# Optimization experiments

Hardware: AMD Instinct MI355X
Metric: run time of the kernel (lower is better)

The kernel has to match this reference:

```python
import jax, jax.numpy as jnp
import numpy as np

H = 16       # num_attention_heads
HKV = 4      # num_key_value_heads
D = 128      # head_dim
CHUNK = 64   # input_chunk_size
RBS = 64     # retrieval_block_size


def setup_inputs() -> dict:
    key = jax.random.key(0)
    ks = jax.random.split(key, 9)
    B, S, HID = 1, 2048, 2048
    RLEN = 2048  # retrieval_block_num * RBS = (S // CHUNK) * RBS
    inv = 0.02
    return {
        "hidden_states": jax.random.normal(ks[0], (B, S, HID), jnp.float32),
        "cos": jax.random.uniform(ks[1], (B, S, D), jnp.float32),
        "sin": jax.random.uniform(ks[2], (B, S, D), jnp.float32),
        "retrieval_k": jax.random.normal(ks[3], (B, HKV, RLEN, D), jnp.float32),
        "retrieval_v": jax.random.normal(ks[4], (B, HKV, RLEN, D), jnp.float32),
        "Wq": jax.random.normal(ks[5], (HID, H * D), jnp.float32) * inv,
        "Wk": jax.random.normal(ks[6], (HID, HKV * D), jnp.float32) * inv,
        "Wv": jax.random.normal(ks[7], (HID, HKV * D), jnp.float32) * inv,
        "Wo": jax.random.normal(ks[8], (H * D, HID), jnp.float32) * inv,
    }


def _rope(x, cos, sin):
    # x: [B, h, S, D]; cos/sin: [B, S, D] (HF apply_rotary_pos_emb, unsqueeze head dim)
    c = cos[:, None, :, :]
    s = sin[:, None, :, :]
    x1, x2 = jnp.split(x, 2, axis=-1)
    rot = jnp.concatenate([-x2, x1], axis=-1)
    return x * c + rot * s


def reference(hidden_states, cos, sin, retrieval_k, retrieval_v, Wq, Wk, Wv, Wo):
    B, S, HID = hidden_states.shape
    G = H // HKV
    scale = D ** -0.5

    q = (hidden_states @ Wq).reshape(B, S, H, D).transpose(0, 2, 1, 3)    # [B,H,S,D]
    k = (hidden_states @ Wk).reshape(B, S, HKV, D).transpose(0, 2, 1, 3)  # [B,HKV,S,D]
    v = (hidden_states @ Wv).reshape(B, S, HKV, D).transpose(0, 2, 1, 3)

    q = _rope(q, cos, sin)
    k = _rope(k, cos, sin)

    # GQA: expand kv heads
    k_full = jnp.repeat(k, G, axis=1)  # [B,H,S,D]
    v_full = jnp.repeat(v, G, axis=1)

    # ---- causal part over input keys ----
    s1 = jnp.einsum('bhqd,bhkd->bhqk', q, k_full) * scale
    causal = jnp.tril(jnp.ones((S, S), bool))
    s1 = jnp.where(causal[None, None], s1, -jnp.inf)

    # ---- retrieval part: chunk c attends retrieval block (c-1) only ----
    C = S // CHUNK
    R = retrieval_k.shape[2] // RBS
    rK = retrieval_k.reshape(B, HKV, R, RBS, D)
    rV = retrieval_v.reshape(B, HKV, R, RBS, D)
    blk_idx = jnp.clip(jnp.arange(C) - 1, 0, R - 1)          # chunk 0 masked below
    rK_sel = jnp.repeat(rK[:, :, blk_idx], G, axis=1)        # [B,H,C,RBS,D]
    rV_sel = jnp.repeat(rV[:, :, blk_idx], G, axis=1)
    qc = q.reshape(B, H, C, CHUNK, D)
    s2 = jnp.einsum('bhcqd,bhckd->bhcqk', qc, rK_sel) * scale
    valid = (jnp.arange(C) >= 1)[None, None, :, None, None]
    s2 = jnp.where(valid, s2, -jnp.inf)

    # ---- joint (numerically stable) softmax over causal + retrieval keys ----
    m1 = jnp.max(s1, axis=-1)                                # [B,H,S]
    m2 = jnp.max(s2, axis=-1).reshape(B, H, S)               # -inf for chunk 0
    m = jnp.maximum(m1, m2)
    e1 = jnp.exp(s1 - m[..., None])
    e2 = jnp.exp(s2 - m.reshape(B, H, C, CHUNK)[..., None])
    denom = e1.sum(-1) + e2.sum(-1).reshape(B, H, S)         # [B,H,S]
    o1 = jnp.einsum('bhqk,bhkd->bhqd', e1, v_full)
    o2 = jnp.einsum('bhcqk,bhckd->bhcqd', e2, rV_sel).reshape(B, H, S, D)
    attn = (o1 + o2) / denom[..., None]                      # [B,H,S,D]

    out = attn.transpose(0, 2, 1, 3).reshape(B, S, H * D)
    return out @ Wo
```

## Files before the change

### kernel.cpp

```cpp
#include <hip/hip_runtime.h>
#include <stdint.h>

#define H_    16
#define HKV_  4
#define D_    128
#define S_    2048
#define HID_  2048
#define RLEN_ 2048

typedef unsigned short u16;
typedef __attribute__((ext_vector_type(4))) float f32x4;
typedef __attribute__((ext_vector_type(16))) float f32x16;
typedef __attribute__((ext_vector_type(8))) __bf16 bf16x8;
typedef __attribute__((ext_vector_type(4))) unsigned short u16x4;
typedef __attribute__((ext_vector_type(8))) unsigned short u16x8;
typedef __attribute__((ext_vector_type(2))) unsigned int u32x2;

__device__ __forceinline__ u16 f2bf(float f) {
  union { float f; unsigned u; } v; v.f = f;
  unsigned r = v.u + 0x7FFFu + ((v.u >> 16) & 1u);
  return (u16)(r >> 16);
}
__device__ __forceinline__ float bf2f(u16 h) {
  union { unsigned u; float f; } v; v.u = ((unsigned)h) << 16;
  return v.f;
}
__device__ __forceinline__ float exp2v(float x) {
  float r; asm("v_exp_f32 %0, %1" : "=v"(r) : "v"(x)); return r;
}
__device__ __forceinline__ unsigned cvtpk(float lo, float hi) {
  unsigned r; asm("v_cvt_pk_bf16_f32 %0, %1, %2" : "=v"(r) : "v"(lo), "v"(hi)); return r;
}
__device__ __forceinline__ void pl32swap(unsigned &a, unsigned &b) {
  u32x2 r = __builtin_amdgcn_permlane32_swap(a, b, false, false);
  a = r.x; b = r.y;
}
__device__ __forceinline__ float xhalf_max(float v) {
  unsigned a = __float_as_uint(v), b = a;
  pl32swap(a, b);
  return fmaxf(__uint_as_float(a), __uint_as_float(b));
}
__device__ __forceinline__ float xhalf_add(float v) {
  unsigned a = __float_as_uint(v), b = a;
  pl32swap(a, b);
  return __uint_as_float(a) + __uint_as_float(b);
}

#define GLL(srcp, ldsp) \
  __builtin_amdgcn_global_load_lds((const __attribute__((address_space(1))) unsigned int*)(srcp), \
                                   (__attribute__((address_space(3))) unsigned int*)(ldsp), 16, 0, 0)

__global__ void k_cvt(const float* __restrict__ in, u16* __restrict__ out, int n4) {
  int i = blockIdx.x * 256 + threadIdx.x;
  if (i >= n4) return;
  float4 v = ((const float4*)in)[i];
  u16x4 o;
  o.x = f2bf(v.x); o.y = f2bf(v.y); o.z = f2bf(v.z); o.w = f2bf(v.w);
  ((u16x4*)out)[i] = o;
}

__global__ void k_transw(const float* __restrict__ in, u16* __restrict__ out, int K, int N) {
  __shared__ float tile[32][33];
  int bx = blockIdx.x * 32, by = blockIdx.y * 32;
  int tx = threadIdx.x, ty = threadIdx.y;
#pragma unroll
  for (int i = 0; i < 32; i += 8)
    tile[ty + i][tx] = in[(size_t)(by + ty + i) * N + bx + tx];
  __syncthreads();
#pragma unroll
  for (int i = 0; i < 32; i += 8)
    out[(size_t)(bx + ty + i) * K + by + tx] = f2bf(tile[tx][ty + i]);
}

__global__ __launch_bounds__(256) void k_gemm(const u16* __restrict__ A, const u16* __restrict__ Bt,
                                              u16* __restrict__ Cb, int M, int N, int K, int Khalf) {
  __shared__ __attribute__((aligned(16))) u16 As[128 * 32];
  __shared__ __attribute__((aligned(16))) u16 Bs[128 * 32];
  const int bm = blockIdx.y * 128, bn = blockIdx.x * 128;
  const int kz0 = blockIdx.z * Khalf, kz1 = kz0 + Khalf;
  u16* C = Cb + (size_t)blockIdx.z * M * N;
  const int tid = threadIdx.x, wave = tid >> 6, lane = tid & 63;
  const int wr = wave >> 1, wc = wave & 1;
  const int l15 = lane & 15, lhi = lane >> 4;
  f32x4 acc[4][4] = {};
  const u16* pA  = A  + (size_t)(bm + (tid >> 2)) * K + (tid & 3) * 8;
  const u16* pA2 = A  + (size_t)(bm + 64 + (tid >> 2)) * K + (tid & 3) * 8;
  const u16* pB  = Bt + (size_t)(bn + (tid >> 2)) * K + (tid & 3) * 8;
  const u16* pB2 = Bt + (size_t)(bn + 64 + (tid >> 2)) * K + (tid & 3) * 8;

  for (int k0 = kz0; k0 < kz1; k0 += 32) {
    __syncthreads();
    GLL(pA + k0,  As + wave * 512);
    GLL(pA2 + k0, As + 2048 + wave * 512);
    GLL(pB + k0,  Bs + wave * 512);
    GLL(pB2 + k0, Bs + 2048 + wave * 512);
    __syncthreads();
    bf16x8 af[4], bfr[4];
#pragma unroll
    for (int m = 0; m < 4; m++)
      af[m] = *(const bf16x8*)(As + (wr * 64 + m * 16 + l15) * 32 + lhi * 8);
#pragma unroll
    for (int n = 0; n < 4; n++)
      bfr[n] = *(const bf16x8*)(Bs + (wc * 64 + n * 16 + l15) * 32 + lhi * 8);
#pragma unroll
    for (int m = 0; m < 4; m++)
#pragma unroll
      for (int n = 0; n < 4; n++)
        acc[m][n] = __builtin_amdgcn_mfma_f32_16x16x32_bf16(af[m], bfr[n], acc[m][n], 0, 0, 0);
  }
  const int r0 = bm + wr * 64, c0 = bn + wc * 64;
#pragma unroll
  for (int m = 0; m < 4; m++)
#pragma unroll
    for (int n = 0; n < 4; n++) {
      int r = r0 + m * 16 + lhi * 4, cc = c0 + n * 16 + l15;
#pragma unroll
      for (int j = 0; j < 4; j++)
        C[(size_t)(r + j) * N + cc] = f2bf(acc[m][n][j]);
    }
}

__global__ void k_comb2(const u16* __restrict__ c0, const u16* __restrict__ c1,
                        float* __restrict__ out, int n8) {
  int i = blockIdx.x * 256 + threadIdx.x;
  if (i >= n8) return;
  u16x8 a = ((const u16x8*)c0)[i];
  u16x8 b = ((const u16x8*)c1)[i];
  float4 o0, o1;
  o0.x = bf2f(a[0]) + bf2f(b[0]); o0.y = bf2f(a[1]) + bf2f(b[1]);
  o0.z = bf2f(a[2]) + bf2f(b[2]); o0.w = bf2f(a[3]) + bf2f(b[3]);
  o1.x = bf2f(a[4]) + bf2f(b[4]); o1.y = bf2f(a[5]) + bf2f(b[5]);
  o1.z = bf2f(a[6]) + bf2f(b[6]); o1.w = bf2f(a[7]) + bf2f(b[7]);
  ((float4*)out)[i * 2]     = o0;
  ((float4*)out)[i * 2 + 1] = o1;
}

__global__ void k_ropeq(const u16* __restrict__ qp0, const float* __restrict__ cs,
                        const float* __restrict__ sn, u16* __restrict__ Q) {
  const u16* qp1 = qp0 + (size_t)2048 * 3072;
  int tid = threadIdx.x;
  int idx = blockIdx.x * 4 + (tid >> 6);
  int d = tid & 63;
  int h = idx >> 11, s = idx & (S_ - 1);
  size_t base = (size_t)s * 3072 + h * 128;
  float x1 = bf2f(qp0[base + d])      + bf2f(qp1[base + d]);
  float x2 = bf2f(qp0[base + d + 64]) + bf2f(qp1[base + d + 64]);
  float c1 = cs[s * D_ + d], s1v = sn[s * D_ + d];
  float c2 = cs[s * D_ + d + 64], s2v = sn[s * D_ + d + 64];
  const float sc = 0.12751744422f;
  u16* o = Q + ((size_t)h * S_ + s) * D_;
  o[d]      = f2bf((x1 * c1 - x2 * s1v) * sc);
  o[d + 64] = f2bf((x2 * c2 + x1 * s2v) * sc);
}

__global__ void k_ropekv(const u16* __restrict__ qp0, const float* __restrict__ cs,
                         const float* __restrict__ sn, u16* __restrict__ Ksw,
                         u16* __restrict__ Vt) {
  const u16* qp1 = qp0 + (size_t)2048 * 3072;
  int tid = threadIdx.x;
  int idx = blockIdx.x * 4 + (tid >> 6);
  int d = tid & 63;
  int kv = idx >> 11, s = idx & (S_ - 1);
  size_t kb = (size_t)s * 3072 + 2048 + kv * 128;
  size_t vb = kb + 512;
  float x1 = bf2f(qp0[kb + d])      + bf2f(qp1[kb + d]);
  float x2 = bf2f(qp0[kb + d + 64]) + bf2f(qp1[kb + d + 64]);
  float v1 = bf2f(qp0[vb + d])      + bf2f(qp1[vb + d]);
  float v2 = bf2f(qp0[vb + d + 64]) + bf2f(qp1[vb + d + 64]);
  float c1 = cs[s * D_ + d], s1v = sn[s * D_ + d];
  float c2 = cs[s * D_ + d + 64], s2v = sn[s * D_ + d + 64];
  u16* ko = Ksw + ((size_t)kv * S_ + s) * D_;
  int sw = (s & 7) << 3;
  ko[d ^ sw]        = f2bf(x1 * c1 - x2 * s1v);
  ko[(d + 64) ^ sw] = f2bf(x2 * c2 + x1 * s2v);
  u16* vo = Vt + (size_t)kv * D_ * S_;
  vo[(size_t)d * S_        + s] = f2bf(v1);
  vo[(size_t)(d + 64) * S_ + s] = f2bf(v2);
}

__global__ void k_retr(const float* __restrict__ rk, const float* __restrict__ rv,
                       u16* __restrict__ Krs, u16* __restrict__ Vtr) {
  int tid = threadIdx.x;
  int idx = blockIdx.x * 2 + (tid >> 7);
  int d = tid & 127;
  int kv = idx >> 11, r = idx & (RLEN_ - 1);
  size_t base = ((size_t)kv * RLEN_ + r) * D_;
  Krs[base + (d ^ ((r & 7) << 3))] = f2bf(rk[base + d]);
  Vtr[((size_t)kv * D_ + d) * RLEN_ + r] = f2bf(rv[base + d]);
}

__global__ __launch_bounds__(256) void k_attn(
    const u16* __restrict__ Q, const u16* __restrict__ Ksw, const u16* __restrict__ Vt,
    const u16* __restrict__ Krs, const u16* __restrict__ Vtr,
    u16* __restrict__ Opart, float* __restrict__ Ml) {
  __shared__ __attribute__((aligned(16))) char smem[69632];
  u16* KlB = (u16*)smem;
  u16* VlB = (u16*)(smem + 32768);
  float* mrg = (float*)smem;

  const int e = 83 - blockIdx.x, h = blockIdx.y, kvh = h >> 2;
  int c, part, np;
  if (e < 7)       { c = e;               part = 0;           np = 1; }
  else if (e < 23) { c = 7 + ((e - 7) >> 1);  part = (e - 7) & 1;  np = 2; }
  else if (e < 47) { c = 15 + (e - 23) / 3;   part = (e - 23) % 3; np = 3; }
  else if (e < 79) { c = 23 + ((e - 47) >> 2); part = (e - 47) & 3; np = 4; }
  else             { c = 31;              part = e - 79;      np = 5; }
  const int nt = (c == 0) ? 1 : (c + 2);
  const int t0 = (part * nt) / np, t1 = ((part + 1) * nt) / np;
  const int bp = h * 84 + e;

  const int tid = threadIdx.x, wave = tid >> 6, lane = tid & 63;
  const int qs = wave & 1, kp = wave >> 1;
  const int l31 = lane & 31, hf = lane >> 5;
  const int qrow = c * 64 + qs * 32 + l31;

  bf16x8 qf[8];
  {
    const u16* qp = Q + ((size_t)h * S_ + qrow) * D_ + hf * 8;
#pragma unroll
    for (int m = 0; m < 8; m++) qf[m] = *(const bf16x8*)(qp + m * 16);
  }
  float mq = -1e30f, lq = 0.f;
  f32x16 accO[4] = {};

  auto tsrc = [&](int t, const u16*& kb, const u16*& vb, int& vstr, int& k0) {
    const bool r_ = (t == c + 1);
    kb = r_ ? (Krs + (size_t)kvh * RLEN_ * D_) : (Ksw + (size_t)kvh * S_ * D_);
    vb = r_ ? (Vtr + (size_t)kvh * D_ * RLEN_) : (Vt + (size_t)kvh * D_ * S_);
    vstr = r_ ? RLEN_ : S_;
    k0 = r_ ? (c - 1) * 64 : t * 64;
  };
  u16x8 vreg[4];
  auto stage_issue = [&](int t, int buf) {
    const u16 *kb, *vb; int vstr, k0;
    tsrc(t, kb, vb, vstr, k0);
#pragma unroll
    for (int p2 = 0; p2 < 4; p2++) {
      int t2 = p2 * 256 + tid;
      GLL(kb + (size_t)(k0 + (t2 >> 4)) * D_ + (t2 & 15) * 8,
          KlB + buf * 8192 + p2 * 2048 + wave * 512);
    }
#pragma unroll
    for (int i = 0; i < 4; i++) {
      int idx = i * 256 + tid;
      vreg[i] = *(const u16x8*)(vb + (size_t)(idx >> 3) * vstr + k0 + (idx & 7) * 8);
    }
  };
  auto stage_write = [&](int buf) {
    u16* vd = VlB + buf * 9216;
#pragma unroll
    for (int i = 0; i < 4; i++) {
      int idx = i * 256 + tid;
      *(u16x8*)(vd + (idx >> 3) * 72 + (idx & 7) * 8) = vreg[i];
    }
  };

  stage_issue(t0, 0);
  stage_write(0);
  __syncthreads();

  for (int t = t0; t < t1; t++) {
    const int cur = (t - t0) & 1;
    const bool isr = (t == c + 1);
    const bool pf = (t + 1 < t1);
    if (pf) stage_issue(t + 1, cur ^ 1);

    f32x16 sacc = {};
    {
      const char* Kbuf = (const char*)(KlB + cur * 8192);
#pragma unroll
      for (int m = 0; m < 8; m++) {
        int by = ((kp * 32 + l31) << 8) + ((m * 32 + hf * 16) ^ ((l31 & 7) << 4));
        bf16x8 kf = *(const bf16x8*)(Kbuf + by);
        sacc = __builtin_amdgcn_mfma_f32_32x32x16_bf16(kf, qf[m], sacc, 0, 0, 0);
      }
    }
    if (!isr && t == c) {
      const int koff = (kp - qs) * 32;
#pragma unroll
      for (int r = 0; r < 16; r++) {
        int kloc = (r & 3) + 8 * (r >> 2) + 4 * hf + koff;
        if (kloc > l31) sacc[r] = -1e30f;
      }
    }
    float tmax = sacc[0];
#pragma unroll
    for (int r = 1; r < 16; r++) tmax = fmaxf(tmax, sacc[r]);
    tmax = xhalf_max(tmax);
    if (!__all(tmax - mq <= 11.5f)) {
      float mn = fmaxf(mq, tmax);
      float f = exp2v(mq - mn);
      mq = mn; lq *= f;
#pragma unroll
      for (int dt = 0; dt < 4; dt++)
#pragma unroll
        for (int r = 0; r < 16; r++) accO[dt][r] *= f;
    }
    float ps = 0.f;
#pragma unroll
    for (int r = 0; r < 16; r++) {
      float p = exp2v(sacc[r] - mq);
      sacc[r] = p; ps += p;
    }
    lq += xhalf_add(ps);
    unsigned W[8];
#pragma unroll
    for (int g = 0; g < 4; g++) {
      W[2 * g]     = cvtpk(sacc[4 * g],     sacc[4 * g + 1]);
      W[2 * g + 1] = cvtpk(sacc[4 * g + 2], sacc[4 * g + 3]);
    }
    const char* Vbuf = (const char*)VlB + cur * 18432;
    __builtin_amdgcn_s_setprio(1);
#pragma unroll
    for (int st = 0; st < 2; st++) {
      unsigned x0 = W[4 * st], y0 = W[4 * st + 2];
      unsigned x1 = W[4 * st + 1], y1 = W[4 * st + 3];
      pl32swap(x0, y0);
      pl32swap(x1, y1);
      union { unsigned u[4]; bf16x8 v; } pfr;
      pfr.u[0] = x0; pfr.u[1] = x1; pfr.u[2] = y0; pfr.u[3] = y1;
#pragma unroll
      for (int dt = 0; dt < 4; dt++) {
        bf16x8 vf = *(const bf16x8*)(Vbuf + (dt * 32 + l31) * 144 + kp * 64 + st * 32 + hf * 16);
        accO[dt] = __builtin_amdgcn_mfma_f32_32x32x16_bf16(vf, pfr.v, accO[dt], 0, 0, 0);
      }
    }
    __builtin_amdgcn_s_setprio(0);
    if (pf) stage_write(cur ^ 1);
    __syncthreads();
  }

  if (kp == 1) {
    float* mb = mrg + qs * 4352 + lane * 68;
#pragma unroll
    for (int dt = 0; dt < 4; dt++)
#pragma unroll
      for (int j = 0; j < 4; j++) {
        f32x4 v4 = {accO[dt][4 * j], accO[dt][4 * j + 1], accO[dt][4 * j + 2], accO[dt][4 * j + 3]};
        *(f32x4*)(mb + dt * 16 + j * 4) = v4;
      }
    mb[64] = mq; mb[65] = lq;
  }
  __syncthreads();
  if (kp == 0) {
    const float* mb = mrg + qs * 4352 + lane * 68;
    float m1 = mb[64], l1 = mb[65];
    float mm = fmaxf(mq, m1);
    float w0 = exp2v(mq - mm), w1 = exp2v(m1 - mm);
    float ll = w0 * lq + w1 * l1;
    u16* op = Opart + (size_t)bp * 8192 + (size_t)(qs * 32 + l31) * 128;
#pragma unroll
    for (int dt = 0; dt < 4; dt++)
#pragma unroll
      for (int j = 0; j < 4; j++) {
        u16x4 o;
#pragma unroll
        for (int b = 0; b < 4; b++)
          o[b] = f2bf(w0 * accO[dt][4 * j + b] + w1 * mb[dt * 16 + 4 * j + b]);
        *(u16x4*)(op + dt * 32 + j * 8 + hf * 4) = o;
      }
    if (hf == 0) {
      Ml[(size_t)bp * 128 + qs * 32 + l31]      = mm;
      Ml[(size_t)bp * 128 + 64 + qs * 32 + l31] = ll;
    }
  }
}

__global__ __launch_bounds__(256) void k_combine(const u16* __restrict__ Opart,
                                                 const float* __restrict__ Ml,
                                                 u16* __restrict__ attn) {
  const int c = blockIdx.x, h = blockIdx.y;
  const int t = threadIdx.x;
  const int q = t >> 2, d0 = (t & 3) * 32;
  int base, np;
  if (c < 7)       { base = c;                 np = 1; }
  else if (c < 15) { base = 7 + 2 * (c - 7);   np = 2; }
  else if (c < 23) { base = 23 + 3 * (c - 15); np = 3; }
  else if (c < 31) { base = 47 + 4 * (c - 23); np = 4; }
  else             { base = 79;                np = 5; }
  const size_t pb = (size_t)h * 84 + base;

  float m = -1e30f;
  for (int p = 0; p < np; p++) m = fmaxf(m, Ml[(pb + p) * 128 + q]);
  float l = 0.f;
  float N[32];
#pragma unroll
  for (int i = 0; i < 32; i++) N[i] = 0.f;
  for (int p = 0; p < np; p++) {
    const float mp = Ml[(pb + p) * 128 + q];
    const float lp = Ml[(pb + p) * 128 + 64 + q];
    const float w = exp2v(mp - m);
    l += w * lp;
    const u16* op = Opart + (pb + p) * 8192 + q * 128 + d0;
#pragma unroll
    for (int i = 0; i < 4; i++) {
      u16x8 v = ((const u16x8*)op)[i];
#pragma unroll
      for (int ee = 0; ee < 8; ee++) N[i * 8 + ee] += w * bf2f(v[ee]);
    }
  }
  const float inv = 1.f / l;
  u16* dst = attn + (size_t)(c * 64 + q) * (H_ * D_) + h * 128 + d0;
#pragma unroll
  for (int i = 0; i < 4; i++) {
    u16x8 o;
#pragma unroll
    for (int ee = 0; ee < 8; ee++) o[ee] = f2bf(N[i * 8 + ee] * inv);
    ((u16x8*)dst)[i] = o;
  }
}

extern "C" void kernel_launch(void* const* d_in, const int* in_sizes, int n_in,
                              void* d_out, int out_size, void* d_ws, size_t ws_size,
                              hipStream_t stream) {
  const float* hs = (const float*)d_in[0];
  const float* cs = (const float*)d_in[1];
  const float* sn = (const float*)d_in[2];
  const float* rk = (const float*)d_in[3];
  const float* rv = (const float*)d_in[4];
  const float* Wq = (const float*)d_in[5];
  const float* Wk = (const float*)d_in[6];
  const float* Wv = (const float*)d_in[7];
  const float* Wo = (const float*)d_in[8];
  float* out = (float*)d_out;
  char* ws = (char*)d_ws;
  if (ws_size < (size_t)(56u << 20)) return;

  u16* hsb  = (u16*)(ws);
  u16* wto  = (u16*)(ws + (8u << 20));
  u16* wtq  = (u16*)(ws + (16u << 20));
  u16* qkvP = (u16*)(ws + (28u << 20));
  u16* Krs  = (u16*)(ws + (52u << 20));
  u16* Vtrs = (u16*)(ws + (54u << 20));
  u16* Qr   = (u16*)(ws + (16u << 20));
  u16* Ks   = (u16*)(ws + (24u << 20));
  u16* Vts  = (u16*)(ws + (26u << 20));
  u16* Opart= (u16*)(ws + (28u << 20));
  float* Ml = (float*)(ws + (49u << 20));
  u16* Cp   = (u16*)(ws + (28u << 20));
  u16* attn = hsb;

  k_cvt<<<4096, 256, 0, stream>>>(hs, hsb, 1048576);
  dim3 tb(32, 8);
  k_transw<<<dim3(64, 64), tb, 0, stream>>>(Wq, wtq, 2048, 2048);
  k_transw<<<dim3(16, 64), tb, 0, stream>>>(Wk, wtq + (size_t)2048 * 2048, 2048, 512);
  k_transw<<<dim3(16, 64), tb, 0, stream>>>(Wv, wtq + (size_t)2560 * 2048, 2048, 512);
  k_transw<<<dim3(64, 64), tb, 0, stream>>>(Wo, wto, 2048, 2048);
  k_gemm<<<dim3(24, 16, 2), 256, 0, stream>>>(hsb, wtq, qkvP, 2048, 3072, 2048, 1024);
  k_ropeq<<<8192, 256, 0, stream>>>(qkvP, cs, sn, Qr);
  k_ropekv<<<2048, 256, 0, stream>>>(qkvP, cs, sn, Ks, Vts);
  k_retr<<<4096, 256, 0, stream>>>(rk, rv, Krs, Vtrs);
  k_attn<<<dim3(84, 16), 256, 0, stream>>>(Qr, Ks, Vts, Krs, Vtrs, Opart, Ml);
  k_combine<<<dim3(32, 16), 256, 0, stream>>>(Opart, Ml, attn);
  k_gemm<<<dim3(16, 16, 2), 256, 0, stream>>>(attn, wto, Cp, 2048, 2048, 2048, 1024);
  k_comb2<<<2048, 256, 0, stream>>>(Cp, Cp + (size_t)2048 * 2048, out, 524288);
}
```

Before: 183.0 us.

## Single-buffer K/V LDS staging to raise attention kernel occupancy

Replaces the double-buffered K/V shared-memory staging in the attention kernel with a single buffer, halving LDS use, and adds a launch-bounds hint for four blocks per CU. K for the next tile is now loaded after a mid-iteration barrier, and V is held in registers and written after the PV step. Per-thread load and store offsets are precomputed and the tile source pointer is advanced incrementally instead of being recomputed. The goal is more resident blocks per CU to hide latency, at the cost of an extra barrier per tile and less overlap between loads and compute inside a block.

```diff
diff --git a/kernel.cpp b/kernel.cpp
--- a/kernel.cpp
+++ b/kernel.cpp
@@ -189,13 +189,13 @@
   Vtr[((size_t)kv * D_ + d) * RLEN_ + r] = f2bf(rv[base + d]);
 }
 
-__global__ __launch_bounds__(256) void k_attn(
+__global__ __launch_bounds__(256, 4) void k_attn(
     const u16* __restrict__ Q, const u16* __restrict__ Ksw, const u16* __restrict__ Vt,
     const u16* __restrict__ Krs, const u16* __restrict__ Vtr,
     u16* __restrict__ Opart, float* __restrict__ Ml) {
-  __shared__ __attribute__((aligned(16))) char smem[69632];
-  u16* KlB = (u16*)smem;
-  u16* VlB = (u16*)(smem + 32768);
+  __shared__ __attribute__((aligned(16))) char smem[34816];
+  u16* Kl = (u16*)smem;
+  u16* Vl = (u16*)(smem + 16384);
   float* mrg = (float*)smem;
 
   const int e = 83 - blockIdx.x, h = blockIdx.y, kvh = h >> 2;
@@ -223,51 +223,47 @@
   float mq = -1e30f, lq = 0.f;
   f32x16 accO[4] = {};
 
-  auto tsrc = [&](int t, const u16*& kb, const u16*& vb, int& vstr, int& k0) {
-    const bool r_ = (t == c + 1);
-    kb = r_ ? (Krs + (size_t)kvh * RLEN_ * D_) : (Ksw + (size_t)kvh * S_ * D_);
-    vb = r_ ? (Vtr + (size_t)kvh * D_ * RLEN_) : (Vt + (size_t)kvh * D_ * S_);
-    vstr = r_ ? RLEN_ : S_;
-    k0 = r_ ? (c - 1) * 64 : t * 64;
-  };
+  int koff[4], voff[4];
+  u16 *kdst[4];
+  int vdst[4];
+#pragma unroll
+  for (int p = 0; p < 4; p++) {
+    koff[p] = p * 2048 + (tid >> 4) * 128 + (tid & 15) * 8;
+    kdst[p] = Kl + p * 2048 + wave * 512;
+  }
+#pragma unroll
+  for (int i = 0; i < 4; i++) {
+    voff[i] = (i * 32 + (tid >> 3)) * 2048 + (tid & 7) * 8;
+    vdst[i] = (i * 32 + (tid >> 3)) * 72 + (tid & 7) * 8;
+  }
+
+  const int cm1 = (c >= 1) ? (c - 1) : 0;
+  const u16* krb = Krs + (size_t)kvh * RLEN_ * D_ + (size_t)cm1 * 64 * D_;
+  const u16* vrb = Vtr + (size_t)kvh * D_ * RLEN_ + cm1 * 64;
+  const u16* kst = Ksw + (size_t)kvh * S_ * D_ + (size_t)t0 * 64 * D_;
+  const u16* vst = Vt + (size_t)kvh * D_ * S_ + t0 * 64;
+  int ts = t0;
+
   u16x8 vreg[4];
-  auto stage_issue = [&](int t, int buf) {
-    const u16 *kb, *vb; int vstr, k0;
-    tsrc(t, kb, vb, vstr, k0);
-#pragma unroll
-    for (int p2 = 0; p2 < 4; p2++) {
-      int t2 = p2 * 256 + tid;
-      GLL(kb + (size_t)(k0 + (t2 >> 4)) * D_ + (t2 & 15) * 8,
-          KlB + buf * 8192 + p2 * 2048 + wave * 512);
-    }
-#pragma unroll
-    for (int i = 0; i < 4; i++) {
-      int idx = i * 256 + tid;
-      vreg[i] = *(const u16x8*)(vb + (size_t)(idx >> 3) * vstr + k0 + (idx & 7) * 8);
-    }
-  };
-  auto stage_write = [&](int buf) {
-    u16* vd = VlB + buf * 9216;
-#pragma unroll
-    for (int i = 0; i < 4; i++) {
-      int idx = i * 256 + tid;
-      *(u16x8*)(vd + (idx >> 3) * 72 + (idx & 7) * 8) = vreg[i];
-    }
-  };
-
-  stage_issue(t0, 0);
-  stage_write(0);
+#pragma unroll
+  for (int p = 0; p < 4; p++) GLL(kst + koff[p], kdst[p]);
+#pragma unroll
+  for (int i = 0; i < 4; i++) vreg[i] = *(const u16x8*)(vst + voff[i]);
+#pragma unroll
+  for (int i = 0; i < 4; i++) *(u16x8*)(Vl + vdst[i]) = vreg[i];
+  ts = t0 + 1;
+  if (ts == c + 1) { kst = krb; vst = vrb; } else { kst += 64 * D_; vst += 64; }
   __syncthreads();
 
   for (int t = t0; t < t1; t++) {
-    const int cur = (t - t0) & 1;
-    const bool isr = (t == c + 1);
     const bool pf = (t + 1 < t1);
-    if (pf) stage_issue(t + 1, cur ^ 1);
-
+    if (pf) {
+#pragma unroll
+      for (int i = 0; i < 4; i++) vreg[i] = *(const u16x8*)(vst + voff[i]);
+    }
     f32x16 sacc = {};
     {
-      const char* Kbuf = (const char*)(KlB + cur * 8192);
+      const char* Kbuf = (const char*)Kl;
 #pragma unroll
       for (int m = 0; m < 8; m++) {
         int by = ((kp * 32 + l31) << 8) + ((m * 32 + hf * 16) ^ ((l31 & 7) << 4));
@@ -275,11 +271,16 @@
         sacc = __builtin_amdgcn_mfma_f32_32x32x16_bf16(kf, qf[m], sacc, 0, 0, 0);
       }
     }
-    if (!isr && t == c) {
-      const int koff = (kp - qs) * 32;
+    __syncthreads();
+    if (pf) {
+#pragma unroll
+      for (int p = 0; p < 4; p++) GLL(kst + koff[p], kdst[p]);
+    }
+    if (t == c) {
+      const int koffm = (kp - qs) * 32;
 #pragma unroll
       for (int r = 0; r < 16; r++) {
-        int kloc = (r & 3) + 8 * (r >> 2) + 4 * hf + koff;
+        int kloc = (r & 3) + 8 * (r >> 2) + 4 * hf + koffm;
         if (kloc > l31) sacc[r] = -1e30f;
       }
     }
@@ -309,7 +310,7 @@
       W[2 * g]     = cvtpk(sacc[4 * g],     sacc[4 * g + 1]);
       W[2 * g + 1] = cvtpk(sacc[4 * g + 2], sacc[4 * g + 3]);
     }
-    const char* Vbuf = (const char*)VlB + cur * 18432;
+    const char* Vbuf = (const char*)Vl;
     __builtin_amdgcn_s_setprio(1);
 #pragma unroll
     for (int st = 0; st < 2; st++) {
@@ -326,10 +327,16 @@
       }
     }
     __builtin_amdgcn_s_setprio(0);
-    if (pf) stage_write(cur ^ 1);
     __syncthreads();
-  }
-
+    if (pf) {
+#pragma unroll
+      for (int i = 0; i < 4; i++) *(u16x8*)(Vl + vdst[i]) = vreg[i];
+      ts++;
+      if (ts == c + 1) { kst = krb; vst = vrb; } else { kst += 64 * D_; vst += 64; }
+    }
+  }
+
+  __syncthreads();
   if (kp == 1) {
     float* mb = mrg + qs * 4352 + lane * 68;
 #pragma unroll
```

After: 236.5 us. 1.29x slower.
